# Performance work log

Hardware: AMD Instinct MI355X
Metric: run time of the kernel (lower is better)

## Reference

```python
import jax, jax.numpy as jnp
import numpy as np

EPS_RMS = 1e-6
EPS_L2 = 1e-12  # torch F.normalize default eps


def _l2_normalize(x):
    n = jnp.sqrt(jnp.sum(x * x, axis=-1, keepdims=True))
    return x / jnp.maximum(n, EPS_L2)


def _dwconv(x, w, b):
    # depthwise Conv1d: x [B,L,D], w [D,1,K], b [D]; padding=K//2 (same length for odd K)
    K = w.shape[-1]
    y = jax.lax.conv_general_dilated(
        jnp.swapaxes(x, 1, 2), w, window_strides=(1,),
        padding=[(K // 2, K // 2)], feature_group_count=w.shape[0],
        dimension_numbers=('NCH', 'OIH', 'NCH'))
    return jnp.swapaxes(y + b[None, :, None], 1, 2)


def setup_inputs() -> dict:
    key = jax.random.key(0)
    ks = jax.random.split(key, 12)
    B, L, D, K = 8, 2048, 128, 3
    inp = {
        'x': jax.random.normal(ks[0], (B, L, D), dtype=jnp.float32),
        'state': jnp.zeros((B, D, D), dtype=jnp.float32),
        'W_in': jax.random.normal(ks[1], (4 * D, D), dtype=jnp.float32) * 0.02,
        'W_gate': jax.random.normal(ks[2], (2 * D, D), dtype=jnp.float32) * 0.02,
        'W_out': jax.random.normal(ks[3], (D, D), dtype=jnp.float32) * 0.02,
        'W_res': jax.random.normal(ks[4], (D, D), dtype=jnp.float32) * 0.02,
        'qconv_w': jax.random.normal(ks[5], (D, 1, K), dtype=jnp.float32) * 0.5,
        'qconv_b': jnp.zeros((D,), dtype=jnp.float32),
        'kconv_w': jax.random.normal(ks[6], (D, 1, K), dtype=jnp.float32) * 0.5,
        'kconv_b': jnp.zeros((D,), dtype=jnp.float32),
        'rms_w': jnp.ones((D,), dtype=jnp.float32),
    }
    return inp


def reference(x, state, W_in, W_gate, W_out, W_res,
              qconv_w, qconv_b, kconv_w, kconv_b, rms_w):
    B, L, D = x.shape
    residual = x @ W_res.T
    qkv = x @ W_in.T  # [B,L,4D]
    q, k, v, gate = jnp.split(qkv, 4, axis=-1)
    q = _l2_normalize(jax.nn.sigmoid(_dwconv(q, qconv_w, qconv_b)))
    k = _l2_normalize(jax.nn.sigmoid(_dwconv(k, kconv_w, kconv_b)))
    g = jax.nn.sigmoid(gate @ W_gate.T)  # [B,L,2D]
    alpha, beta = jnp.split(g, 2, axis=-1)

    # Delta-rule recurrence over time. State S [B,D,D] indexed S[b, v_dim, k_dim]:
    # S <- alpha_j * (S_ij - (S k)_i * beta_j k_j) + beta_j * v_i k_j ; out = silu(q @ S)
    def step(S, inp):
        q_t, k_t, v_t, a_t, b_t = inp  # each [B,D]
        Sk = jnp.einsum('bij,bj->bi', S, k_t)          # S @ k
        bk = b_t * k_t                                  # beta*k, column scaling
        S = a_t[:, None, :] * (S - Sk[:, :, None] * bk[:, None, :]) \
            + v_t[:, :, None] * bk[:, None, :]
        out_t = jax.nn.silu(jnp.einsum('bi,bij->bj', q_t, S))
        return S, out_t

    xs = tuple(jnp.swapaxes(a, 0, 1) for a in (q, k, v, alpha, beta))  # [L,B,D]
    S_fin, outs = jax.lax.scan(step, state, xs)
    out = jnp.swapaxes(outs, 0, 1) @ W_out.T  # [B,L,D]
    # dropout (p=0.125) is identity in eval mode
    out = out * jax.lax.rsqrt(jnp.mean(out * out, axis=-1, keepdims=True) + EPS_RMS) * rms_w
    out = out + residual
    return out, S_fin
```

## Files before the change

### kernel.cpp

```cpp
#include <hip/hip_runtime.h>
#include <hip/hip_bf16.h>
#include <math.h>

#define BB 8
#define LL 2048
#define LQ 512
#define DD 128

template <int CTRL>
__device__ __forceinline__ float dpp_add(float x) {
    int xi = __float_as_int(x);
    int yi = __builtin_amdgcn_update_dpp(xi, xi, CTRL, 0xF, 0xF, false);
    return x + __int_as_float(yi);
}
__device__ __forceinline__ float allreduce16(float p) {
    p = dpp_add<0xB1>(p);
    p = dpp_add<0x4E>(p);
    p = dpp_add<0x141>(p);
    p = dpp_add<0x140>(p);
    return p;
}
__device__ __forceinline__ float red_tail(float p) {
    p += __int_as_float(__builtin_amdgcn_ds_swizzle(__float_as_int(p), 0x401F));
    p += __shfl_xor(p, 32);
    return p;
}

__global__ __launch_bounds__(256) void gemm_kernel(
    const float* __restrict__ X, long ldx, long sB, long sQ,
    const float* __restrict__ W,
    float* __restrict__ C, int ldc,
    int applySig)
{
    __shared__ float Xs[32 * 132];
    __shared__ float Ws[64 * 132];
    const int tid = threadIdx.x;
    const int m0 = blockIdx.x * 32;
    const int o0 = blockIdx.y * 64;
    {
        int row = tid >> 3, cg = tid & 7;
        int m = m0 + row;
        int b = m >> 11, t = m & 2047, qq = t >> 9, tl = t & 511;
        const float* src = X + (size_t)b * sB + (size_t)qq * sQ
                             + (size_t)tl * ldx + cg * 16;
        float* dst = Xs + row * 132 + cg * 16;
#pragma unroll
        for (int u = 0; u < 4; ++u)
            *(float4*)(dst + 4 * u) = *(const float4*)(src + 4 * u);
    }
    {
        int o = tid >> 2, cg = tid & 3;
        const float* src = W + (size_t)(o0 + o) * 128 + cg * 32;
        float* dst = Ws + o * 132 + cg * 32;
#pragma unroll
        for (int u = 0; u < 8; ++u)
            *(float4*)(dst + 4 * u) = *(const float4*)(src + 4 * u);
    }
    __syncthreads();
    const int tx = tid & 31, ty = tid >> 5;
    float acc[4][2] = {};
    const float* xb = Xs + (ty * 4) * 132;
    const float* wb = Ws + (tx * 2) * 132;
    for (int k0 = 0; k0 < 128; k0 += 4) {
        float4 xr[4], wr[2];
#pragma unroll
        for (int r = 0; r < 4; ++r) xr[r] = *(const float4*)(xb + r * 132 + k0);
#pragma unroll
        for (int cc = 0; cc < 2; ++cc) wr[cc] = *(const float4*)(wb + cc * 132 + k0);
#pragma unroll
        for (int r = 0; r < 4; ++r)
#pragma unroll
            for (int cc = 0; cc < 2; ++cc) {
                acc[r][cc] += xr[r].x * wr[cc].x + xr[r].y * wr[cc].y
                            + xr[r].z * wr[cc].z + xr[r].w * wr[cc].w;
            }
    }
#pragma unroll
    for (int r = 0; r < 4; ++r)
#pragma unroll
        for (int cc = 0; cc < 2; ++cc) {
            float v = acc[r][cc];
            if (applySig) v = 1.0f / (1.0f + __expf(-v));
            C[(size_t)(m0 + ty * 4 + r) * ldc + o0 + tx * 2 + cc] = v;
        }
}

__global__ __launch_bounds__(256) void convnorm_kernel(
    const float* __restrict__ qkv,
    const float* __restrict__ qw, const float* __restrict__ qb,
    const float* __restrict__ kw, const float* __restrict__ kb,
    const float* __restrict__ ab,
    float* __restrict__ pack)
{
    const int tid = threadIdx.x;
    const int lane = tid & 63;
    const int wid = tid >> 6;
    const int m = blockIdx.x * 4 + wid;
    const int l = m & (LL - 1);
    const int b = m >> 11;
    const int d0 = lane * 2;
    float yq0 = qb[d0], yq1 = qb[d0 + 1];
    float yk0 = kb[d0], yk1 = kb[d0 + 1];
#pragma unroll
    for (int tau = 0; tau < 3; ++tau) {
        int lp = l + tau - 1;
        if (lp >= 0 && lp < LL) {
            const float* base = qkv + (size_t)(m + tau - 1) * 512;
            yq0 += base[d0]       * qw[d0 * 3 + tau];
            yq1 += base[d0 + 1]   * qw[(d0 + 1) * 3 + tau];
            yk0 += base[128 + d0]     * kw[d0 * 3 + tau];
            yk1 += base[128 + d0 + 1] * kw[(d0 + 1) * 3 + tau];
        }
    }
    yq0 = 1.0f / (1.0f + __expf(-yq0));
    yq1 = 1.0f / (1.0f + __expf(-yq1));
    yk0 = 1.0f / (1.0f + __expf(-yk0));
    yk1 = 1.0f / (1.0f + __expf(-yk1));
    float sq = yq0 * yq0 + yq1 * yq1;
    float sk = yk0 * yk0 + yk1 * yk1;
#pragma unroll
    for (int msk = 1; msk <= 32; msk <<= 1) {
        sq += __shfl_xor(sq, msk);
        sk += __shfl_xor(sk, msk);
    }
    float rq = 1.0f / fmaxf(sqrtf(sq), 1e-12f);
    float rk = 1.0f / fmaxf(sqrtf(sk), 1e-12f);
    float k0n = yk0 * rk, k1n = yk1 * rk;
    float a0 = ab[(size_t)m * 256 + d0];
    float a1 = ab[(size_t)m * 256 + d0 + 1];
    float b0 = ab[(size_t)m * 256 + 128 + d0];
    float b1 = ab[(size_t)m * 256 + 128 + d0 + 1];
    float v0 = qkv[(size_t)m * 512 + 256 + d0];
    float v1 = qkv[(size_t)m * 512 + 256 + d0 + 1];
    float* P = pack + ((size_t)b * 512 + (l >> 2)) * 2560 + (l & 3);
    P[d0 * 4]              = k0n;      P[(d0 + 1) * 4]        = k1n;
    P[512 + d0 * 4]        = b0 * k0n; P[512 + (d0 + 1) * 4]  = b1 * k1n;
    P[1024 + d0 * 4]       = a0;       P[1024 + (d0 + 1) * 4] = a1;
    P[1536 + d0 * 4]       = yq0 * rq; P[1536 + (d0 + 1) * 4] = yq1 * rq;
    P[2048 + d0 * 4]       = v0;       P[2048 + (d0 + 1) * 4] = v1;
}

__global__ __launch_bounds__(256) void blockprep_kernel(
    float* __restrict__ pack, float* __restrict__ gh)
{
    const int lane = threadIdx.x & 63;
    const int w = threadIdx.x >> 6;
    const int tbid = blockIdx.x * 4 + w;
    const int j0 = lane * 2;
    float* P = pack + (size_t)tbid * 2560;
    float4 kc[2], mc[2], ac[2];
    kc[0] = *(const float4*)(P + j0 * 4);
    kc[1] = *(const float4*)(P + j0 * 4 + 4);
    mc[0] = *(const float4*)(P + 512 + j0 * 4);
    mc[1] = *(const float4*)(P + 512 + j0 * 4 + 4);
    ac[0] = *(const float4*)(P + 1024 + j0 * 4);
    ac[1] = *(const float4*)(P + 1024 + j0 * 4 + 4);
    float s[12];
#pragma unroll
    for (int i = 0; i < 12; ++i) s[i] = 0.f;
#pragma unroll
    for (int c = 0; c < 2; ++c) {
        const float k1 = kc[c].y, k2 = kc[c].z, k3 = kc[c].w;
        const float m0 = mc[c].x, m1 = mc[c].y, m2 = mc[c].z;
        const float a0 = ac[c].x, a1 = ac[c].y, a2 = ac[c].z;
        float t  = m0, ta = a0 * m0;
        s[0]  += t * k1;   s[1]  += ta * k1;
        t *= a1; ta *= a1;
        s[2]  += t * k2;   s[3]  += ta * k2;
        t *= a2; ta *= a2;
        s[4]  += t * k3;   s[5]  += ta * k3;
        float u = m1, ua = a1 * m1;
        s[6]  += u * k2;   s[7]  += ua * k2;
        u *= a2; ua *= a2;
        s[8]  += u * k3;   s[9]  += ua * k3;
        s[10] += m2 * k3;  s[11] += a2 * m2 * k3;
        const float p01 = a0, p012 = a0 * a1;
        kc[c].y = k1 * p01;
        kc[c].z = k2 * p012;
        kc[c].w = k3 * (p012 * a2);
    }
#pragma unroll
    for (int i = 0; i < 12; ++i)
#pragma unroll
        for (int msk = 1; msk <= 32; msk <<= 1)
            s[i] += __shfl_xor(s[i], msk);
    *(float4*)(P + j0 * 4)     = kc[0];
    *(float4*)(P + j0 * 4 + 4) = kc[1];
    if (lane == 0) {
        float* q = gh + (size_t)tbid * 16;
        float4 g0 = { s[0], s[1], s[2],  s[3]  };
        float4 g1 = { s[4], s[5], s[6],  s[7]  };
        float4 g2 = { s[8], s[9], s[10], s[11] };
        *(float4*)(q)     = g0;
        *(float4*)(q + 4) = g1;
        *(float4*)(q + 8) = g2;
    }
}

__global__ __launch_bounds__(64, 1) void recur1_kernel(
    const float* __restrict__ pack, const float* __restrict__ ghg,
    const float* __restrict__ sin,
    __hip_bfloat16* __restrict__ pout, float* __restrict__ sout, int blk0)
{
    const int lane = threadIdx.x;
    const int b = blockIdx.x >> 7;
    const int g = blockIdx.x & 127;
    const int j0 = lane * 2;

    float SA[2];
    {
        const float* sp = sin + ((size_t)b * DD + g) * DD + j0;
        float2 t2 = *(const float2*)sp;
        SA[0] = t2.x; SA[1] = t2.y;
    }

    const float* P  = pack + ((size_t)b * 512 + blk0) * 2560;
    const float* GH = ghg  + ((size_t)b * 512 + blk0) * 16;
    __hip_bfloat16* po = pout + ((size_t)g * (BB * LQ) + (size_t)b * LQ) * DD + j0;

    float4 ka[2][2], ma[2][2], aa[2][2], qv[2], vv[2], gA[2], gB[2], gC[2];

#define PREB(BF)                                                             \
    do {                                                                     \
        ka[BF][0] = *(const float4*)(P + j0 * 4);                            \
        ka[BF][1] = *(const float4*)(P + j0 * 4 + 4);                        \
        ma[BF][0] = *(const float4*)(P + 512 + j0 * 4);                      \
        ma[BF][1] = *(const float4*)(P + 512 + j0 * 4 + 4);                  \
        aa[BF][0] = *(const float4*)(P + 1024 + j0 * 4);                     \
        aa[BF][1] = *(const float4*)(P + 1024 + j0 * 4 + 4);                 \
        qv[BF]    = *(const float4*)(P + 1536 + g * 4);                      \
        vv[BF]    = *(const float4*)(P + 2048 + g * 4);                      \
        gA[BF]    = *(const float4*)(GH);                                    \
        gB[BF]    = *(const float4*)(GH + 4);                                \
        gC[BF]    = *(const float4*)(GH + 8);                                \
        P += 2560; GH += 16;                                                 \
        __builtin_amdgcn_sched_barrier(0);         \
    } while (0)

#define UPD(BF, CMP, SK)                                                     \
    do {                                                                     \
        const float a0 = aa[BF][0].CMP, a1 = aa[BF][1].CMP;                  \
        const float m0 = ma[BF][0].CMP, m1 = ma[BF][1].CMP;                  \
        const float vg = vv[BF].CMP, qg = qv[BF].CMP;                        \
        float w0 = fmaf(-a0, SK, vg);                                        \
        SA[0] = fmaf(m0, w0, a0 * SA[0]);                                    \
        float w1 = fmaf(-a1, SK, vg);                                        \
        SA[1] = fmaf(m1, w1, a1 * SA[1]);                                    \
        __hip_bfloat162 h2;                                                  \
        h2.x = __float2bfloat16(qg * SA[0]);                                 \
        h2.y = __float2bfloat16(qg * SA[1]);                                 \
        *(__hip_bfloat162*)po = h2;                                          \
        po += DD;                                                            \
    } while (0)

#define BLOCK(BF)                                                            \
    do {                                                                     \
        float E0 = fmaf(SA[1], ka[BF][1].x, SA[0] * ka[BF][0].x);            \
        float E1 = fmaf(SA[1], ka[BF][1].y, SA[0] * ka[BF][0].y);            \
        float E2 = fmaf(SA[1], ka[BF][1].z, SA[0] * ka[BF][0].z);            \
        float E3 = fmaf(SA[1], ka[BF][1].w, SA[0] * ka[BF][0].w);            \
        E0 = allreduce16(E0); E1 = allreduce16(E1);                          \
        E2 = allreduce16(E2); E3 = allreduce16(E3);                          \
        E0 = red_tail(E0); E1 = red_tail(E1);                                \
        E2 = red_tail(E2); E3 = red_tail(E3);                                \
        const float vg0 = vv[BF].x, vg1 = vv[BF].y, vg2 = vv[BF].z;          \
        float u1 = vg0 * gA[BF].x;                                           \
        float u2 = fmaf(vg1, gB[BF].z, vg0 * gA[BF].z);                      \
        float u3 = fmaf(vg2, gC[BF].z, fmaf(vg1, gC[BF].x, vg0 * gB[BF].x)); \
        float sk0 = E0;                                                      \
        float sk1 = fmaf(-sk0, gA[BF].y, E1 + u1);                           \
        float sk2 = fmaf(-sk1, gB[BF].w, fmaf(-sk0, gA[BF].w, E2 + u2));     \
        float sk3 = fmaf(-sk2, gC[BF].w,                                     \
                    fmaf(-sk1, gC[BF].y, fmaf(-sk0, gB[BF].y, E3 + u3)));    \
        UPD(BF, x, sk0); UPD(BF, y, sk1); UPD(BF, z, sk2); UPD(BF, w, sk3);  \
    } while (0)

    PREB(0);
    PREB(1);
    for (int tb = 0; tb < LQ / 4; tb += 2) {
        BLOCK(0);
        PREB(0);
        BLOCK(1);
        PREB(1);
    }
#undef PREB
#undef UPD
#undef BLOCK

    {
        float* sp = sout + ((size_t)b * DD + g) * DD + j0;
        float2 o2 = {SA[0], SA[1]};
        *(float2*)sp = o2;
    }
}

__global__ __launch_bounds__(256) void combine_silu_kernel(
    const ushort* __restrict__ pout, float* __restrict__ ocbase, int q)
{
    const size_t NQ = (size_t)BB * LQ * DD;
    size_t idx = ((size_t)blockIdx.x * 256 + threadIdx.x) * 4;
    float s0 = 0, s1 = 0, s2 = 0, s3 = 0;
#pragma unroll 8
    for (int gi = 0; gi < 128; ++gi) {
        uint2 u = *(const uint2*)(pout + gi * NQ + idx);
        s0 += __uint_as_float((u.x & 0xffffu) << 16);
        s1 += __uint_as_float(u.x & 0xffff0000u);
        s2 += __uint_as_float((u.y & 0xffffu) << 16);
        s3 += __uint_as_float(u.y & 0xffff0000u);
    }
    float4 r;
    r.x = s0 / (1.0f + __expf(-s0));
    r.y = s1 / (1.0f + __expf(-s1));
    r.z = s2 / (1.0f + __expf(-s2));
    r.w = s3 / (1.0f + __expf(-s3));
    size_t b = idx >> 16;
    size_t rem = idx & ((size_t)LQ * DD - 1);
    float* dst = ocbase + b * (512ull * 2560) + (size_t)q * (128ull * 2560) + rem;
    *(float4*)dst = r;
}

__global__ __launch_bounds__(256) void rms_res_kernel(
    const float* __restrict__ y, const float* __restrict__ res,
    const float* __restrict__ rmsw, float* __restrict__ out)
{
    const int tid = threadIdx.x;
    const int lane = tid & 63;
    const int wid = tid >> 6;
    const int m = blockIdx.x * 4 + wid;
    const int d0 = lane * 2;
    size_t o = (size_t)m * DD + d0;
    float2 yv = *(const float2*)(y + o);
    float ss = yv.x * yv.x + yv.y * yv.y;
#pragma unroll
    for (int msk = 1; msk <= 32; msk <<= 1) ss += __shfl_xor(ss, msk);
    float r = rsqrtf(ss * (1.0f / 128.0f) + 1e-6f);
    float2 rv = *(const float2*)(res + o);
    out[o]     = yv.x * r * rmsw[d0]     + rv.x;
    out[o + 1] = yv.y * r * rmsw[d0 + 1] + rv.y;
}

extern "C" void kernel_launch(void* const* d_in, const int* in_sizes, int n_in,
                              void* d_out, int out_size, void* d_ws, size_t ws_size,
                              hipStream_t stream)
{
    const float* x      = (const float*)d_in[0];
    const float* state  = (const float*)d_in[1];
    const float* W_in   = (const float*)d_in[2];
    const float* W_gate = (const float*)d_in[3];
    const float* W_out  = (const float*)d_in[4];
    const float* W_res  = (const float*)d_in[5];
    const float* qcw    = (const float*)d_in[6];
    const float* qcb    = (const float*)d_in[7];
    const float* kcw    = (const float*)d_in[8];
    const float* kcb    = (const float*)d_in[9];
    const float* rmsw   = (const float*)d_in[10];
    float* out  = (float*)d_out;
    float* sfin = out + (size_t)BB * LL * DD;
    float* ghs  = out;

    const size_t M = (size_t)BB * LL;
    char* base = (char*)d_ws;
    const size_t PACK_BYTES = M * 640 * 4;
    float* pack = (float*)base;
    char*  poreg = base + PACK_BYTES;
    float* qkv = (float*)poreg;
    float* abv = (float*)(poreg + M * 512 * 4);
    __hip_bfloat16* po = (__hip_bfloat16*)poreg;
    float* res = (float*)poreg;
    float* yb  = (float*)(poreg + M * DD * 4);

    dim3 blk(256);
    gemm_kernel<<<dim3(M / 32, 8), blk, 0, stream>>>(
        x, 128, 2048L * 128, 512L * 128, W_in, qkv, 512, 0);
    gemm_kernel<<<dim3(M / 32, 4), blk, 0, stream>>>(
        qkv + 384, 512, 2048L * 512, 512L * 512, W_gate, abv, 256, 1);
    convnorm_kernel<<<dim3(M / 4), blk, 0, stream>>>(qkv, qcw, qcb, kcw, kcb, abv, pack);
    blockprep_kernel<<<dim3(1024), blk, 0, stream>>>(pack, ghs);
    for (int q = 0; q < 4; ++q) {
        const float* sin = (q == 0) ? state : sfin;
        recur1_kernel<<<dim3(BB * 128), dim3(64), 0, stream>>>(
            pack, ghs, sin, po, sfin, q * 128);
        combine_silu_kernel<<<dim3(512), blk, 0, stream>>>(
            (const ushort*)po, pack, q);
    }
    gemm_kernel<<<dim3(M / 32, 2), blk, 0, stream>>>(
        x, 128, 2048L * 128, 512L * 128, W_res, res, 128, 0);
    gemm_kernel<<<dim3(M / 32, 2), blk, 0, stream>>>(
        pack, 128, 512L * 2560, 128L * 2560, W_out, yb, 128, 0);
    rms_res_kernel<<<dim3(M / 4), blk, 0, stream>>>(yb, res, rmsw, out);
}
```

Baseline: 577.9 us.

## Stage recurrence k/m/a operands through LDS with async global_load_lds ring buffer

The recurrence kernel now streams its per-block k, m and a vectors into a four-deep LDS ring using global_load_lds, and reads them back from LDS. Only the q, v and gate values are still loaded directly into registers. An explicit vmcnt wait keeps three blocks of loads in flight. The goal is deeper prefetch of the serial recurrence's operands without the register pressure of double-buffered float4 arrays. In exchange it adds LDS read latency, and correctness depends on a hand-tuned vmcnt count.

```diff
diff --git a/kernel.cpp b/kernel.cpp
--- a/kernel.cpp
+++ b/kernel.cpp
@@ -25,6 +25,12 @@
     p += __shfl_xor(p, 32);
     return p;
 }
+
+#define GLDS(GP, LP)                                                          \
+    __builtin_amdgcn_global_load_lds(                                         \
+        (const __attribute__((address_space(1))) unsigned int*)(const void*)(GP), \
+        (__attribute__((address_space(3))) unsigned int*)(void*)(LP),         \
+        16, 0, 0)
 
 __global__ __launch_bounds__(256) void gemm_kernel(
     const float* __restrict__ X, long ldx, long sB, long sQ,
@@ -202,94 +208,112 @@
     const float* __restrict__ sin,
     __hip_bfloat16* __restrict__ pout, float* __restrict__ sout, int blk0)
 {
+    __shared__ float ldsb[4][1536];
     const int lane = threadIdx.x;
     const int b = blockIdx.x >> 7;
     const int g = blockIdx.x & 127;
     const int j0 = lane * 2;
 
-    float SA[2];
+    float SA0, SA1;
     {
         const float* sp = sin + ((size_t)b * DD + g) * DD + j0;
         float2 t2 = *(const float2*)sp;
-        SA[0] = t2.x; SA[1] = t2.y;
+        SA0 = t2.x; SA1 = t2.y;
     }
 
     const float* P  = pack + ((size_t)b * 512 + blk0) * 2560;
     const float* GH = ghg  + ((size_t)b * 512 + blk0) * 16;
     __hip_bfloat16* po = pout + ((size_t)g * (BB * LQ) + (size_t)b * LQ) * DD + j0;
 
-    float4 ka[2][2], ma[2][2], aa[2][2], qv[2], vv[2], gA[2], gB[2], gC[2];
-
-#define PREB(BF)                                                             \
+    const float* ps = P;
+    const float* pu = P;
+
+    float4 uqA, uvA, gAA, gBA, gCA;
+    float4 uqB, uvB, gAB, gBB, gCB;
+
+#define STAGE(BUF)                                                           \
     do {                                                                     \
-        ka[BF][0] = *(const float4*)(P + j0 * 4);                            \
-        ka[BF][1] = *(const float4*)(P + j0 * 4 + 4);                        \
-        ma[BF][0] = *(const float4*)(P + 512 + j0 * 4);                      \
-        ma[BF][1] = *(const float4*)(P + 512 + j0 * 4 + 4);                  \
-        aa[BF][0] = *(const float4*)(P + 1024 + j0 * 4);                     \
-        aa[BF][1] = *(const float4*)(P + 1024 + j0 * 4 + 4);                 \
-        qv[BF]    = *(const float4*)(P + 1536 + g * 4);                      \
-        vv[BF]    = *(const float4*)(P + 2048 + g * 4);                      \
-        gA[BF]    = *(const float4*)(GH);                                    \
-        gB[BF]    = *(const float4*)(GH + 4);                                \
-        gC[BF]    = *(const float4*)(GH + 8);                                \
-        P += 2560; GH += 16;                                                 \
-        __builtin_amdgcn_sched_barrier(0);         \
+        GLDS(ps + j0 * 4,              &ldsb[BUF][0]);                       \
+        GLDS(ps + j0 * 4 + 4,          &ldsb[BUF][256]);                     \
+        GLDS(ps + 512 + j0 * 4,        &ldsb[BUF][512]);                     \
+        GLDS(ps + 512 + j0 * 4 + 4,    &ldsb[BUF][768]);                     \
+        GLDS(ps + 1024 + j0 * 4,       &ldsb[BUF][1024]);                    \
+        GLDS(ps + 1024 + j0 * 4 + 4,   &ldsb[BUF][1280]);                    \
+        ps += 2560;                                                          \
     } while (0)
 
-#define UPD(BF, CMP, SK)                                                     \
+#define ULOAD(SUF)                                                           \
     do {                                                                     \
-        const float a0 = aa[BF][0].CMP, a1 = aa[BF][1].CMP;                  \
-        const float m0 = ma[BF][0].CMP, m1 = ma[BF][1].CMP;                  \
-        const float vg = vv[BF].CMP, qg = qv[BF].CMP;                        \
-        float w0 = fmaf(-a0, SK, vg);                                        \
-        SA[0] = fmaf(m0, w0, a0 * SA[0]);                                    \
-        float w1 = fmaf(-a1, SK, vg);                                        \
-        SA[1] = fmaf(m1, w1, a1 * SA[1]);                                    \
+        uq##SUF = *(const float4*)(pu + 1536 + g * 4);                       \
+        uv##SUF = *(const float4*)(pu + 2048 + g * 4);                       \
+        gA##SUF = *(const float4*)(GH);                                      \
+        gB##SUF = *(const float4*)(GH + 4);                                  \
+        gC##SUF = *(const float4*)(GH + 8);                                  \
+        pu += 2560; GH += 16;                                                \
+    } while (0)
+
+#define UPD(U, CMP, SK)                                                      \
+    do {                                                                     \
+        float w0 = fmaf(-aa0.CMP, SK, uv##U.CMP);                            \
+        SA0 = fmaf(ma0.CMP, w0, aa0.CMP * SA0);                              \
+        float w1 = fmaf(-aa1.CMP, SK, uv##U.CMP);                            \
+        SA1 = fmaf(ma1.CMP, w1, aa1.CMP * SA1);                              \
         __hip_bfloat162 h2;                                                  \
-        h2.x = __float2bfloat16(qg * SA[0]);                                 \
-        h2.y = __float2bfloat16(qg * SA[1]);                                 \
+        h2.x = __float2bfloat16(uq##U.CMP * SA0);                            \
+        h2.y = __float2bfloat16(uq##U.CMP * SA1);                            \
         *(__hip_bfloat162*)po = h2;                                          \
         po += DD;                                                            \
     } while (0)
 
-#define BLOCK(BF)                                                            \
+#define SUB(BUF, U, NU)                                                      \
     do {                                                                     \
-        float E0 = fmaf(SA[1], ka[BF][1].x, SA[0] * ka[BF][0].x);            \
-        float E1 = fmaf(SA[1], ka[BF][1].y, SA[0] * ka[BF][0].y);            \
-        float E2 = fmaf(SA[1], ka[BF][1].z, SA[0] * ka[BF][0].z);            \
-        float E3 = fmaf(SA[1], ka[BF][1].w, SA[0] * ka[BF][0].w);            \
-        E0 = allreduce16(E0); E1 = allreduce16(E1);                          \
-        E2 = allreduce16(E2); E3 = allreduce16(E3);                          \
-        E0 = red_tail(E0); E1 = red_tail(E1);                                \
-        E2 = red_tail(E2); E3 = red_tail(E3);                                \
-        const float vg0 = vv[BF].x, vg1 = vv[BF].y, vg2 = vv[BF].z;          \
-        float u1 = vg0 * gA[BF].x;                                           \
-        float u2 = fmaf(vg1, gB[BF].z, vg0 * gA[BF].z);                      \
-        float u3 = fmaf(vg2, gC[BF].z, fmaf(vg1, gC[BF].x, vg0 * gB[BF].x)); \
+        ULOAD(NU);                               \
+        STAGE((BUF + 3) & 3);       \
+        asm volatile("s_waitcnt vmcnt(18)" ::: "memory");                    \
+        __builtin_amdgcn_sched_barrier(0);                                   \
+        const float4 ka0 = *(const float4*)&ldsb[BUF][lane * 4];             \
+        const float4 ka1 = *(const float4*)&ldsb[BUF][256 + lane * 4];       \
+        const float4 ma0 = *(const float4*)&ldsb[BUF][512 + lane * 4];       \
+        const float4 ma1 = *(const float4*)&ldsb[BUF][768 + lane * 4];       \
+        const float4 aa0 = *(const float4*)&ldsb[BUF][1024 + lane * 4];      \
+        const float4 aa1 = *(const float4*)&ldsb[BUF][1280 + lane * 4];      \
+        float E0 = fmaf(SA1, ka1.x, SA0 * ka0.x);                            \
+        float E1 = fmaf(SA1, ka1.y, SA0 * ka0.y);                            \
+        float E2 = fmaf(SA1, ka1.z, SA0 * ka0.z);                            \
+        float E3 = fmaf(SA1, ka1.w, SA0 * ka0.w);                            \
+        __builtin_amdgcn_sched_barrier(0);                                   \
+        E0 = red_tail(allreduce16(E0));                                      \
+        E1 = red_tail(allreduce16(E1));                                      \
+        E2 = red_tail(allreduce16(E2));                                      \
+        E3 = red_tail(allreduce16(E3));                                      \
+        float u1 = uv##U.x * gA##U.x;                                        \
+        float u2 = fmaf(uv##U.y, gB##U.z, uv##U.x * gA##U.z);                \
+        float u3 = fmaf(uv##U.z, gC##U.z,                                    \
+                   fmaf(uv##U.y, gC##U.x, uv##U.x * gB##U.x));               \
         float sk0 = E0;                                                      \
-        float sk1 = fmaf(-sk0, gA[BF].y, E1 + u1);                           \
-        float sk2 = fmaf(-sk1, gB[BF].w, fmaf(-sk0, gA[BF].w, E2 + u2));     \
-        float sk3 = fmaf(-sk2, gC[BF].w,                                     \
-                    fmaf(-sk1, gC[BF].y, fmaf(-sk0, gB[BF].y, E3 + u3)));    \
-        UPD(BF, x, sk0); UPD(BF, y, sk1); UPD(BF, z, sk2); UPD(BF, w, sk3);  \
+        float sk1 = fmaf(-sk0, gA##U.y, E1 + u1);                            \
+        float sk2 = fmaf(-sk1, gB##U.w, fmaf(-sk0, gA##U.w, E2 + u2));       \
+        float sk3 = fmaf(-sk2, gC##U.w,                                      \
+                    fmaf(-sk1, gC##U.y, fmaf(-sk0, gB##U.y, E3 + u3)));      \
+        UPD(U, x, sk0); UPD(U, y, sk1); UPD(U, z, sk2); UPD(U, w, sk3);      \
     } while (0)
 
-    PREB(0);
-    PREB(1);
-    for (int tb = 0; tb < LQ / 4; tb += 2) {
-        BLOCK(0);
-        PREB(0);
-        BLOCK(1);
-        PREB(1);
-    }
-#undef PREB
+    STAGE(0); STAGE(1); STAGE(2);
+    ULOAD(A);
+    for (int tb = 0; tb < LQ / 4; tb += 4) {
+        SUB(0, A, B);
+        SUB(1, B, A);
+        SUB(2, A, B);
+        SUB(3, B, A);
+    }
+#undef STAGE
+#undef ULOAD
 #undef UPD
-#undef BLOCK
+#undef SUB
 
     {
         float* sp = sout + ((size_t)b * DD + g) * DD + j0;
-        float2 o2 = {SA[0], SA[1]};
+        float2 o2 = {SA0, SA1};
         *(float2*)sp = o2;
     }
 }
```

Result: slower. 722.5 us (+25.0%).

## Split recurrence row across two wavefronts with LDS exchange of partial dots

Applied to the files above, without the earlier changes.

The recurrence kernel now uses 128 threads per state row, one element per thread, instead of one 64-lane wavefront holding two elements each. Each wave reduces its half of the S·k dot products, then the two halves are exchanged through double-buffered shared memory with a __syncthreads per 4-step block. The aim is to halve per-lane serial work and cut the latency of the sequential update chain. The cost is a block-wide barrier and an LDS round trip on every block of the critical path.

```diff
diff --git a/kernel.cpp b/kernel.cpp
--- a/kernel.cpp
+++ b/kernel.cpp
@@ -197,101 +197,92 @@
     }
 }
 
-__global__ __launch_bounds__(64, 1) void recur1_kernel(
+__global__ __launch_bounds__(128, 1) void recur2_kernel(
     const float* __restrict__ pack, const float* __restrict__ ghg,
     const float* __restrict__ sin,
     __hip_bfloat16* __restrict__ pout, float* __restrict__ sout, int blk0)
 {
-    const int lane = threadIdx.x;
+    __shared__ float xch[2][2][4];
+    const int tid = threadIdx.x;
+    const int lane = tid & 63;
+    const int wid = tid >> 6;
     const int b = blockIdx.x >> 7;
     const int g = blockIdx.x & 127;
-    const int j0 = lane * 2;
-
-    float SA[2];
-    {
-        const float* sp = sin + ((size_t)b * DD + g) * DD + j0;
-        float2 t2 = *(const float2*)sp;
-        SA[0] = t2.x; SA[1] = t2.y;
-    }
+
+    float SA = sin[((size_t)b * DD + g) * DD + tid];
 
     const float* P  = pack + ((size_t)b * 512 + blk0) * 2560;
     const float* GH = ghg  + ((size_t)b * 512 + blk0) * 16;
-    __hip_bfloat16* po = pout + ((size_t)g * (BB * LQ) + (size_t)b * LQ) * DD + j0;
-
-    float4 ka[2][2], ma[2][2], aa[2][2], qv[2], vv[2], gA[2], gB[2], gC[2];
+    __hip_bfloat16* po = pout + ((size_t)g * (BB * LQ) + (size_t)b * LQ) * DD + tid;
+
+    float4 ka[2], ma[2], aa[2], qv[2], vv[2], gA[2], gB[2], gC[2];
 
 #define PREB(BF)                                                             \
     do {                                                                     \
-        ka[BF][0] = *(const float4*)(P + j0 * 4);                            \
-        ka[BF][1] = *(const float4*)(P + j0 * 4 + 4);                        \
-        ma[BF][0] = *(const float4*)(P + 512 + j0 * 4);                      \
-        ma[BF][1] = *(const float4*)(P + 512 + j0 * 4 + 4);                  \
-        aa[BF][0] = *(const float4*)(P + 1024 + j0 * 4);                     \
-        aa[BF][1] = *(const float4*)(P + 1024 + j0 * 4 + 4);                 \
-        qv[BF]    = *(const float4*)(P + 1536 + g * 4);                      \
-        vv[BF]    = *(const float4*)(P + 2048 + g * 4);                      \
-        gA[BF]    = *(const float4*)(GH);                                    \
-        gB[BF]    = *(const float4*)(GH + 4);                                \
-        gC[BF]    = *(const float4*)(GH + 8);                                \
+        ka[BF] = *(const float4*)(P + tid * 4);                              \
+        ma[BF] = *(const float4*)(P + 512 + tid * 4);                        \
+        aa[BF] = *(const float4*)(P + 1024 + tid * 4);                       \
+        qv[BF] = *(const float4*)(P + 1536 + g * 4);                         \
+        vv[BF] = *(const float4*)(P + 2048 + g * 4);                         \
+        gA[BF] = *(const float4*)(GH);                                       \
+        gB[BF] = *(const float4*)(GH + 4);                                   \
+        gC[BF] = *(const float4*)(GH + 8);                                   \
         P += 2560; GH += 16;                                                 \
         __builtin_amdgcn_sched_barrier(0);         \
     } while (0)
 
 #define UPD(BF, CMP, SK)                                                     \
     do {                                                                     \
-        const float a0 = aa[BF][0].CMP, a1 = aa[BF][1].CMP;                  \
-        const float m0 = ma[BF][0].CMP, m1 = ma[BF][1].CMP;                  \
-        const float vg = vv[BF].CMP, qg = qv[BF].CMP;                        \
-        float w0 = fmaf(-a0, SK, vg);                                        \
-        SA[0] = fmaf(m0, w0, a0 * SA[0]);                                    \
-        float w1 = fmaf(-a1, SK, vg);                                        \
-        SA[1] = fmaf(m1, w1, a1 * SA[1]);                                    \
-        __hip_bfloat162 h2;                                                  \
-        h2.x = __float2bfloat16(qg * SA[0]);                                 \
-        h2.y = __float2bfloat16(qg * SA[1]);                                 \
-        *(__hip_bfloat162*)po = h2;                                          \
+        const float at = aa[BF].CMP;                                         \
+        float w = fmaf(-at, SK, vv[BF].CMP);                                 \
+        SA = fmaf(ma[BF].CMP, w, at * SA);                                   \
+        *po = __float2bfloat16(qv[BF].CMP * SA);                             \
         po += DD;                                                            \
     } while (0)
 
-#define BLOCK(BF)                                                            \
+#define BLOCK(BF, PAR)                                                       \
     do {                                                                     \
-        float E0 = fmaf(SA[1], ka[BF][1].x, SA[0] * ka[BF][0].x);            \
-        float E1 = fmaf(SA[1], ka[BF][1].y, SA[0] * ka[BF][0].y);            \
-        float E2 = fmaf(SA[1], ka[BF][1].z, SA[0] * ka[BF][0].z);            \
-        float E3 = fmaf(SA[1], ka[BF][1].w, SA[0] * ka[BF][0].w);            \
-        E0 = allreduce16(E0); E1 = allreduce16(E1);                          \
-        E2 = allreduce16(E2); E3 = allreduce16(E3);                          \
-        E0 = red_tail(E0); E1 = red_tail(E1);                                \
-        E2 = red_tail(E2); E3 = red_tail(E3);                                \
+        float E0 = SA * ka[BF].x;                                            \
+        float E1 = SA * ka[BF].y;                                            \
+        float E2 = SA * ka[BF].z;                                            \
+        float E3 = SA * ka[BF].w;                                            \
+        E0 = red_tail(allreduce16(E0));                                      \
+        E1 = red_tail(allreduce16(E1));                                      \
+        E2 = red_tail(allreduce16(E2));                                      \
+        E3 = red_tail(allreduce16(E3));                                      \
+        if (lane == 0) {                                                     \
+            float4 h4 = {E0, E1, E2, E3};                                    \
+            *(float4*)&xch[PAR][wid][0] = h4;                                \
+        }                                                                    \
+        __syncthreads();                                                     \
+        const float4 oth = *(const float4*)&xch[PAR][wid ^ 1][0];            \
+        float F0 = E0 + oth.x, F1 = E1 + oth.y;                              \
+        float F2 = E2 + oth.z, F3 = E3 + oth.w;                              \
         const float vg0 = vv[BF].x, vg1 = vv[BF].y, vg2 = vv[BF].z;          \
         float u1 = vg0 * gA[BF].x;                                           \
         float u2 = fmaf(vg1, gB[BF].z, vg0 * gA[BF].z);                      \
         float u3 = fmaf(vg2, gC[BF].z, fmaf(vg1, gC[BF].x, vg0 * gB[BF].x)); \
-        float sk0 = E0;                                                      \
-        float sk1 = fmaf(-sk0, gA[BF].y, E1 + u1);                           \
-        float sk2 = fmaf(-sk1, gB[BF].w, fmaf(-sk0, gA[BF].w, E2 + u2));     \
+        float sk0 = F0;                                                      \
+        float sk1 = fmaf(-sk0, gA[BF].y, F1 + u1);                           \
+        float sk2 = fmaf(-sk1, gB[BF].w, fmaf(-sk0, gA[BF].w, F2 + u2));     \
         float sk3 = fmaf(-sk2, gC[BF].w,                                     \
-                    fmaf(-sk1, gC[BF].y, fmaf(-sk0, gB[BF].y, E3 + u3)));    \
+                    fmaf(-sk1, gC[BF].y, fmaf(-sk0, gB[BF].y, F3 + u3)));    \
         UPD(BF, x, sk0); UPD(BF, y, sk1); UPD(BF, z, sk2); UPD(BF, w, sk3);  \
     } while (0)
 
     PREB(0);
     PREB(1);
     for (int tb = 0; tb < LQ / 4; tb += 2) {
-        BLOCK(0);
+        BLOCK(0, 0);
         PREB(0);
-        BLOCK(1);
+        BLOCK(1, 1);
         PREB(1);
     }
 #undef PREB
 #undef UPD
 #undef BLOCK
 
-    {
-        float* sp = sout + ((size_t)b * DD + g) * DD + j0;
-        float2 o2 = {SA[0], SA[1]};
-        *(float2*)sp = o2;
-    }
+    sout[((size_t)b * DD + g) * DD + tid] = SA;
 }
 
 __global__ __launch_bounds__(256) void combine_silu_kernel(
@@ -378,7 +369,7 @@
     blockprep_kernel<<<dim3(1024), blk, 0, stream>>>(pack, ghs);
     for (int q = 0; q < 4; ++q) {
         const float* sin = (q == 0) ? state : sfin;
-        recur1_kernel<<<dim3(BB * 128), dim3(64), 0, stream>>>(
+        recur2_kernel<<<dim3(BB * 128), dim3(128), 0, stream>>>(
             pack, ghs, sin, po, sfin, q * 128);
         combine_silu_kernel<<<dim3(512), blk, 0, stream>>>(
             (const ushort*)po, pack, q);
```

Measured after the change: 627.0 us. 8.5% more time.
